# Performance work log

Hardware: AMD Instinct MI355X
Metric: run time of the kernel (lower is better)

Reference implementation:

```python
import jax, jax.numpy as jnp
import numpy as np

B, S, E, L = 8, 2048, 512, 128


def setup_inputs() -> dict:
    key = jax.random.key(0)
    k1, k2 = jax.random.split(key)
    embeddings = jax.random.normal(k1, (B, S, E), dtype=jnp.float32)
    means = jax.random.normal(k2, (L, E), dtype=jnp.float32)
    var = jnp.ones((E,), dtype=jnp.float32)  # default init: requires_grad=False, ones
    return {"embeddings": embeddings, "means": means, "var": var}


def reference(embeddings, means, var):
    # Diagonal-Gaussian log-density per (token, label):
    #   log_density - 0.5 * sum_e (means[l,e] - emb[b,s,e])^2 / var[e]
    # Rewritten as GEMM + per-row/per-label norms (avoids [B,S,L,E] intermediate).
    n_embed = embeddings.shape[-1]
    factor = -n_embed / 2.0 * (np.log(2.0) + np.log(np.pi))
    # After init_params: log_density = factor - 0.5 * sum(log var); var=ones -> factor.
    log_density = factor - 0.5 * jnp.sum(jnp.log(var))
    inv_var = 1.0 / var  # [E]
    e2 = jnp.einsum('bse,e->bs', embeddings * embeddings, inv_var)      # [B,S]
    m2 = jnp.einsum('le,e->l', means * means, inv_var)                  # [L]
    cross = jnp.einsum('bse,le->bsl', embeddings, means * inv_var)      # [B,S,L]
    sq_mahalanobis = e2[..., None] + m2[None, None, :] - 2.0 * cross    # [B,S,L]
    return log_density - 0.5 * sq_mahalanobis
```

## Files before the change

### kernel.cpp

```cpp
#include <hip/hip_runtime.h>
#include <math.h>

#define BDIM 8
#define SDIM 2048
#define EDIM 512
#define LDIM 128
#define MTOT (BDIM * SDIM)

typedef __attribute__((ext_vector_type(8))) short s8v;
typedef __attribute__((ext_vector_type(4))) float f4v;

__device__ __forceinline__ unsigned short f2bf(float x) {
    union { float f; unsigned u; } c; c.f = x;
    return (unsigned short)((c.u + 0x7fffu + ((c.u >> 16) & 1u)) >> 16);
}

__global__ __launch_bounds__(64) void gs_prep(
    const float* __restrict__ means, const float* __restrict__ var,
    unsigned short* __restrict__ Bmat, float* __restrict__ m2,
    float* __restrict__ ivbuf, float* __restrict__ coef)
{
    const int l = blockIdx.x;
    const int t = threadIdx.x;
    const int e0 = t * 8;

    float mv[8], iv[8];
    const float* mrow = means + l * EDIM + e0;
#pragma unroll
    for (int i = 0; i < 8; ++i) { mv[i] = mrow[i]; iv[i] = 1.0f / var[e0 + i]; }

    float part = 0.0f;
    s8v pr;
#pragma unroll
    for (int i = 0; i < 8; ++i) {
        float p = mv[i] * iv[i];
        pr[i] = (short)f2bf(p);
        part += mv[i] * p;
    }
    *(s8v*)(Bmat + l * EDIM + e0) = pr;

#pragma unroll
    for (int off = 32; off > 0; off >>= 1) part += __shfl_down(part, off, 64);
    if (t == 0) m2[l] = part;

    if (l == 0) {
#pragma unroll
        for (int i = 0; i < 8; ++i) ivbuf[e0 + i] = iv[i];
        float ld = 0.0f;
#pragma unroll
        for (int i = 0; i < 8; ++i) ld += logf(var[e0 + i]);
#pragma unroll
        for (int off = 32; off > 0; off >>= 1) ld += __shfl_down(ld, off, 64);
        if (t == 0) {
            const float factor = -(float)EDIM * 0.5f * 1.8378770664093453f;
            *coef = factor - 0.5f * ld;
        }
    }
}

__global__ __launch_bounds__(128) void gs_main(
    const float* __restrict__ emb, const unsigned short* __restrict__ Bmat,
    const float* __restrict__ m2, const float* __restrict__ ivbuf,
    const float* __restrict__ coef, float* __restrict__ out)
{
    const int t    = threadIdx.x;
    const int lane = t & 63;
    const int wave = t >> 6;
    const int q    = lane >> 4;
    const int fr   = lane & 15;
    const int m0   = blockIdx.x * 32 + wave * 16;

    const float*          ap  = emb   + (size_t)(m0 + fr) * EDIM + q * 8;
    const unsigned short* bp  = Bmat  + fr * EDIM + q * 8;
    const float*          ivp = ivbuf + q * 8;

    f4v acc[8];
#pragma unroll
    for (int i = 0; i < 8; ++i) acc[i] = (f4v)0.0f;

    f4v a0[4], a1[4];
    f4v v0[2], v1[2];
    s8v bf[2][8];

#pragma unroll
    for (int p = 0; p < 4; ++p) {
        a0[p] = *(const f4v*)(ap + 32 * p);
        a1[p] = *(const f4v*)(ap + 32 * p + 4);
    }
#pragma unroll
    for (int p = 0; p < 2; ++p) {
        v0[p] = *(const f4v*)(ivp + 32 * p);
        v1[p] = *(const f4v*)(ivp + 32 * p + 4);
#pragma unroll
        for (int ct = 0; ct < 8; ++ct)
            bf[p][ct] = *(const s8v*)(bp + ct * 16 * EDIM + 32 * p);
    }

    float e2acc = 0.0f;

#pragma unroll
    for (int s = 0; s < 16; ++s) {
        f4v xa = a0[s & 3], xb = a1[s & 3];
        f4v va = v0[s & 1], vb = v1[s & 1];
        s8v bcur[8];
#pragma unroll
        for (int ct = 0; ct < 8; ++ct) bcur[ct] = bf[s & 1][ct];

        if (s + 4 < 16) {
            a0[(s + 4) & 3] = *(const f4v*)(ap + 32 * (s + 4));
            a1[(s + 4) & 3] = *(const f4v*)(ap + 32 * (s + 4) + 4);
        }
        if (s + 2 < 16) {
            v0[s & 1] = *(const f4v*)(ivp + 32 * (s + 2));
            v1[s & 1] = *(const f4v*)(ivp + 32 * (s + 2) + 4);
#pragma unroll
            for (int ct = 0; ct < 8; ++ct)
                bf[s & 1][ct] = *(const s8v*)(bp + ct * 16 * EDIM + 32 * (s + 2));
        }

        s8v af;
#pragma unroll
        for (int i = 0; i < 4; ++i) {
            af[i] = (short)f2bf(xa[i]);
            e2acc += xa[i] * xa[i] * va[i];
        }
#pragma unroll
        for (int i = 0; i < 4; ++i) {
            af[4 + i] = (short)f2bf(xb[i]);
            e2acc += xb[i] * xb[i] * vb[i];
        }

#pragma unroll
        for (int ct = 0; ct < 8; ++ct)
            acc[ct] = __builtin_amdgcn_mfma_f32_16x16x32_bf16(af, bcur[ct], acc[ct], 0, 0, 0);
    }

    e2acc += __shfl_xor(e2acc, 16, 64);
    e2acc += __shfl_xor(e2acc, 32, 64);
    float e2row[4];
#pragma unroll
    for (int r = 0; r < 4; ++r) e2row[r] = __shfl(e2acc, q * 4 + r, 64);

    const float cf = *coef;
#pragma unroll
    for (int ct = 0; ct < 8; ++ct) {
        const int n = ct * 16 + fr;
        const float cm = cf - 0.5f * m2[n];
#pragma unroll
        for (int r = 0; r < 4; ++r) {
            const int row = q * 4 + r;
            out[(size_t)(m0 + row) * LDIM + n] = acc[ct][r] + cm - 0.5f * e2row[r];
        }
    }
}

extern "C" void kernel_launch(void* const* d_in, const int* in_sizes, int n_in,
                              void* d_out, int out_size, void* d_ws, size_t ws_size,
                              hipStream_t stream) {
    const float* emb   = (const float*)d_in[0];
    const float* means = (const float*)d_in[1];
    const float* var   = (const float*)d_in[2];
    float* out = (float*)d_out;

    char* ws = (char*)d_ws;
    unsigned short* Bmat = (unsigned short*)ws;
    float* m2    = (float*)(ws + 131072);
    float* ivbuf = (float*)(ws + 131584);
    float* coef  = (float*)(ws + 133632);

    gs_prep<<<LDIM, 64, 0, stream>>>(means, var, Bmat, m2, ivbuf, coef);
    gs_main<<<MTOT / 32, 128, 0, stream>>>(emb, Bmat, m2, ivbuf, coef, out);
}
```

Measured before the change: 94.75 us.

## Stage B matrix in LDS shared across waves instead of per-wave global loads

Each block now cooperatively copies the bf16 means matrix into shared memory in two halves of K, laid out in MFMA fragment order, with barriers between stages. The MFMA loop then reads B fragments from LDS rather than each wave loading them from global/L2 with register double-buffering. This halves redundant B traffic per block and frees registers, but adds barriers, LDS usage (64KB per block, limiting occupancy) and removes the overlap of B loads with compute.

```diff
diff --git a/kernel.cpp b/kernel.cpp
--- a/kernel.cpp
+++ b/kernel.cpp
@@ -1,11 +1,9 @@
 #include <hip/hip_runtime.h>
 #include <math.h>
 
-#define BDIM 8
-#define SDIM 2048
 #define EDIM 512
 #define LDIM 128
-#define MTOT (BDIM * SDIM)
+#define MTOT 16384
 
 typedef __attribute__((ext_vector_type(8))) short s8v;
 typedef __attribute__((ext_vector_type(4))) float f4v;
@@ -63,6 +61,8 @@
     const float* __restrict__ m2, const float* __restrict__ ivbuf,
     const float* __restrict__ coef, float* __restrict__ out)
 {
+    __shared__ __align__(16) unsigned short Blds[64 * 64 * 8];
+
     const int t    = threadIdx.x;
     const int lane = t & 63;
     const int wave = t >> 6;
@@ -70,69 +70,78 @@
     const int fr   = lane & 15;
     const int m0   = blockIdx.x * 32 + wave * 16;
 
-    const float*          ap  = emb   + (size_t)(m0 + fr) * EDIM + q * 8;
-    const unsigned short* bp  = Bmat  + fr * EDIM + q * 8;
-    const float*          ivp = ivbuf + q * 8;
-
-    f4v acc[8];
-#pragma unroll
-    for (int i = 0; i < 8; ++i) acc[i] = (f4v)0.0f;
+    const float* ap  = emb   + (size_t)(m0 + fr) * EDIM + q * 8;
+    const float* ivp = ivbuf + q * 8;
 
     f4v a0[4], a1[4];
-    f4v v0[2], v1[2];
-    s8v bf[2][8];
-
 #pragma unroll
     for (int p = 0; p < 4; ++p) {
         a0[p] = *(const f4v*)(ap + 32 * p);
         a1[p] = *(const f4v*)(ap + 32 * p + 4);
     }
+    f4v v0[2], v1[2];
 #pragma unroll
     for (int p = 0; p < 2; ++p) {
         v0[p] = *(const f4v*)(ivp + 32 * p);
         v1[p] = *(const f4v*)(ivp + 32 * p + 4);
-#pragma unroll
-        for (int ct = 0; ct < 8; ++ct)
-            bf[p][ct] = *(const s8v*)(bp + ct * 16 * EDIM + 32 * p);
     }
 
+    f4v acc[8];
+#pragma unroll
+    for (int i = 0; i < 8; ++i) acc[i] = (f4v)0.0f;
     float e2acc = 0.0f;
 
 #pragma unroll
-    for (int s = 0; s < 16; ++s) {
-        f4v xa = a0[s & 3], xb = a1[s & 3];
-        f4v va = v0[s & 1], vb = v1[s & 1];
-        s8v bcur[8];
-#pragma unroll
-        for (int ct = 0; ct < 8; ++ct) bcur[ct] = bf[s & 1][ct];
-
-        if (s + 4 < 16) {
-            a0[(s + 4) & 3] = *(const f4v*)(ap + 32 * (s + 4));
-            a1[(s + 4) & 3] = *(const f4v*)(ap + 32 * (s + 4) + 4);
+    for (int pass = 0; pass < 2; ++pass) {
+        if (pass) __syncthreads();
+        {
+            const int kb = pass * 256;
+#pragma unroll 16
+            for (int c = 0; c < 32; ++c) {
+                const int fl  = c * 128 + t;
+                const int frg = fl >> 6;
+                const int ln  = fl & 63;
+                const int col = (frg & 7) * 16 + (ln & 15);
+                const int k   = kb + (frg >> 3) * 32 + (ln >> 4) * 8;
+                *(s8v*)&Blds[fl * 8] = *(const s8v*)(Bmat + col * EDIM + k);
+            }
         }
-        if (s + 2 < 16) {
-            v0[s & 1] = *(const f4v*)(ivp + 32 * (s + 2));
-            v1[s & 1] = *(const f4v*)(ivp + 32 * (s + 2) + 4);
-#pragma unroll
-            for (int ct = 0; ct < 8; ++ct)
-                bf[s & 1][ct] = *(const s8v*)(bp + ct * 16 * EDIM + 32 * (s + 2));
-        }
-
-        s8v af;
-#pragma unroll
-        for (int i = 0; i < 4; ++i) {
-            af[i] = (short)f2bf(xa[i]);
-            e2acc += xa[i] * xa[i] * va[i];
-        }
-#pragma unroll
-        for (int i = 0; i < 4; ++i) {
-            af[4 + i] = (short)f2bf(xb[i]);
-            e2acc += xb[i] * xb[i] * vb[i];
-        }
+        __syncthreads();
 
 #pragma unroll
-        for (int ct = 0; ct < 8; ++ct)
-            acc[ct] = __builtin_amdgcn_mfma_f32_16x16x32_bf16(af, bcur[ct], acc[ct], 0, 0, 0);
+        for (int ss = 0; ss < 8; ++ss) {
+            const int s = pass * 8 + ss;
+            f4v xa = a0[s & 3], xb = a1[s & 3];
+            f4v va = v0[s & 1], vb = v1[s & 1];
+
+            if (s + 2 < 16) {
+                v0[s & 1] = *(const f4v*)(ivp + 32 * (s + 2));
+                v1[s & 1] = *(const f4v*)(ivp + 32 * (s + 2) + 4);
+            }
+            if (s + 4 < 16) {
+                a0[s & 3] = *(const f4v*)(ap + 32 * (s + 4));
+                a1[s & 3] = *(const f4v*)(ap + 32 * (s + 4) + 4);
+            }
+
+            s8v af;
+#pragma unroll
+            for (int i = 0; i < 4; ++i) {
+                af[i] = (short)f2bf(xa[i]);
+                e2acc += xa[i] * xa[i] * va[i];
+            }
+#pragma unroll
+            for (int i = 0; i < 4; ++i) {
+                af[4 + i] = (short)f2bf(xb[i]);
+                e2acc += xb[i] * xb[i] * vb[i];
+            }
+
+            const unsigned short* bbase = &Blds[(ss * 8) * 64 * 8 + lane * 8];
+#pragma unroll
+            for (int ct = 0; ct < 8; ++ct) {
+                s8v bfv = *(const s8v*)(bbase + ct * 64 * 8);
+                acc[ct] = __builtin_amdgcn_mfma_f32_16x16x32_bf16(af, bfv, acc[ct], 0, 0, 0);
+            }
+        }
     }
 
     e2acc += __shfl_xor(e2acc, 16, 64);
```

Result: no change. 93.81 us (-1.0%).
